# Kernel tuning notes

Hardware: AMD Instinct MI355X
Metric: run time of the kernel (lower is better)

## Reference

```python
import jax, jax.numpy as jnp
import numpy as np

NEG_BIG = -9e15
ALPHA = 0.2  # LeakyReLU slope


def setup_inputs() -> dict:
    key = jax.random.key(0)
    k1, k2, k3, k4 = jax.random.split(key, 4)
    B, N, Fin, Fout = 8, 2048, 256, 64
    h = jax.random.normal(k1, (B, N, Fin), dtype=jnp.float32)
    adj = jax.random.randint(k2, (B, N, N), 0, 2, dtype=jnp.int32)
    # xavier_uniform-ish scale for W and a
    W = jax.random.normal(k3, (Fin, Fout), dtype=jnp.float32) * (1.414 * np.sqrt(2.0 / (Fin + Fout)))
    a = jax.random.normal(k4, (2 * Fout, 1), dtype=jnp.float32) * (1.414 * np.sqrt(2.0 / (2 * Fout + 1)))
    return {"h": h, "adj": adj, "W": W, "a": a}


def reference(h, adj, W, a):
    Fout = W.shape[1]
    Wh = jnp.einsum("bnf,fo->bno", h, W)  # [B,N,Fout]
    # Decompose concat-based score: a_input @ a == Wh@a1 (src) + Wh@a2 (dst)
    a1, a2 = a[:Fout, 0], a[Fout:, 0]
    e_src = Wh @ a1  # [B,N]
    e_dst = Wh @ a2  # [B,N]
    e = e_src[:, :, None] + e_dst[:, None, :]  # [B,N,N]
    e = jnp.where(e > 0, e, ALPHA * e)  # LeakyReLU
    scores = jnp.where(adj > 0, e, NEG_BIG)
    attention = jax.nn.softmax(scores, axis=-1)  # [B,N,N]
    h_prime = jnp.einsum("bnm,bmo->bno", attention, Wh)
    return jax.nn.elu(h_prime)  # concat=True
```

## Files before the change

### kernel.cpp

```cpp
#include <hip/hip_runtime.h>

#define L2E 1.44269504088896340736f

typedef float f32x4 __attribute__((ext_vector_type(4)));
typedef __bf16 bf16x8 __attribute__((ext_vector_type(8)));
typedef __bf16 bf16x4 __attribute__((ext_vector_type(4)));

__device__ inline void mfma_bf16(bf16x8 a, bf16x8 b, f32x4& c) {
    c = __builtin_amdgcn_mfma_f32_16x16x32_bf16(a, b, c, 0, 0, 0);
}

#define WS_ESRC 2097152
#define WS_EDST 2162688
#define WS_NUM  2228224
#define WS_DEN  6422528
#define WS_MSK  6488064


__global__ __launch_bounds__(256, 8)
void k_msk(const int* __restrict__ adj, unsigned* __restrict__ mask) {
    const int t = blockIdx.x * 256 + threadIdx.x;
    const int4* ap = (const int4*)(adj + (size_t)t * 32);
    int4 q0 = ap[0], q1 = ap[1], q2 = ap[2], q3 = ap[3];
    int4 q4 = ap[4], q5 = ap[5], q6 = ap[6], q7 = ap[7];
    unsigned m = 0u;
#define PK(Q, S)                                                              \
    m |= ((Q.x > 0) ? 1u : 0u) << (S);                                        \
    m |= ((Q.y > 0) ? 1u : 0u) << ((S) + 1);                                  \
    m |= ((Q.z > 0) ? 1u : 0u) << ((S) + 2);                                  \
    m |= ((Q.w > 0) ? 1u : 0u) << ((S) + 3);
    PK(q0, 0) PK(q1, 4) PK(q2, 8) PK(q3, 12)
    PK(q4, 16) PK(q5, 20) PK(q6, 24) PK(q7, 28)
#undef PK
    mask[t] = m;
}

__global__ __launch_bounds__(256, 2)
void k1_wh(const float* __restrict__ h, const float* __restrict__ W,
           const float* __restrict__ a, __bf16* __restrict__ whP,
           float* __restrict__ esrc, float* __restrict__ edst,
           float* __restrict__ numden) {
    const int tid  = threadIdx.x;
    const int lane = tid & 63;
    const int w    = tid >> 6;
    const int blk  = blockIdx.x;
    const int r0   = blk * 8;
    const int b    = r0 >> 11;
    const int n0   = r0 & 2047;

    if (tid < 130) {
        const int zi = blk * 130 + tid;
        *(float4*)&numden[zi * 4] = make_float4(0.f, 0.f, 0.f, 0.f);
    }

    __shared__ float pt_s[8][4][64];
    __shared__ float whs[64][8];

    float wreg[64];
    {
        const float* Wp = W + (size_t)(w * 64) * 64 + lane;
#pragma unroll
        for (int kk = 0; kk < 64; kk++) wreg[kk] = Wp[(size_t)kk * 64];
    }

    const float* hbase = h + (size_t)r0 * 256 + w * 64;
    for (int rr = 0; rr < 8; rr++) {
        const float4* hp = (const float4*)(hbase + rr * 256);
        float acc = 0.f;
#pragma unroll
        for (int q = 0; q < 16; q++) {
            float4 hv = hp[q];
            acc += hv.x * wreg[4 * q + 0];
            acc += hv.y * wreg[4 * q + 1];
            acc += hv.z * wreg[4 * q + 2];
            acc += hv.w * wreg[4 * q + 3];
        }
        pt_s[rr][w][lane] = acc;
    }
    __syncthreads();

    const float a1 = a[lane];
    const float a2 = a[64 + lane];
#pragma unroll
    for (int rq = 0; rq < 2; rq++) {
        const int rr = w * 2 + rq;
        float v = pt_s[rr][0][lane] + pt_s[rr][1][lane] +
                  pt_s[rr][2][lane] + pt_s[rr][3][lane];
        whs[lane][rr] = v;
        float e1 = v * a1, e2 = v * a2;
#pragma unroll
        for (int d = 1; d < 64; d <<= 1) {
            e1 += __shfl_xor(e1, d);
            e2 += __shfl_xor(e2, d);
        }
        if (lane == 0) { esrc[r0 + rr] = e1; edst[r0 + rr] = e2; }
    }
    __syncthreads();

    if (tid < 128) {
        const int o  = tid >> 1, hf = (tid & 1) * 4;
        float4 v = *(const float4*)&whs[o][hf];
        bf16x4 bv = { (__bf16)v.x, (__bf16)v.y, (__bf16)v.z, (__bf16)v.w };
        const int t   = n0 >> 6;
        const int kh  = (n0 >> 5) & 1;
        const int hi2 = (n0 >> 3) & 3;
        const int ob  = o >> 4;
        const int rr  = o & 15;
        const size_t flat =
            ((((size_t)(b * 32 + t) * 2 + kh) * 4 + ob) * 4 + hi2) * 128 +
            rr * 8 + hf;
        *(bf16x4*)(whP + flat) = bv;
    }
}

__global__ __launch_bounds__(512, 2)
void k2_attn(const unsigned* __restrict__ mask, const __bf16* __restrict__ whP,
             const float* __restrict__ esrc, const float* __restrict__ edst,
             float* __restrict__ num, float* __restrict__ den) {
    const int tid  = threadIdx.x;
    const int lane = tid & 63;
    const int w    = tid >> 6;
    const int blk  = blockIdx.x;
    const int b    = blk & 7;
    const int t2   = blk >> 3;
    const int jq   = t2 & 3;
    const int rg   = t2 >> 2;
    const int i0   = rg * 128;
    const int r    = lane & 15;
    const int hi   = lane >> 4;

    __shared__ __align__(16) __bf16 whp_s[32768];
    __shared__ unsigned msk_s[128][18];
    __shared__ float edst_s[512];
    __shared__ float esrc_s[128];
    __shared__ float red_s[8];

    const __bf16* wsrc = whP + (size_t)b * 131072 + (size_t)jq * 32768;
#pragma unroll
    for (int it = 0; it < 8; it++) {
        const int idx = it * 512 + tid;
        *(bf16x8*)&whp_s[idx * 8] = *(const bf16x8*)&wsrc[(size_t)idx * 8];
    }
    const unsigned* mbase = mask + (size_t)(b * 2048 + i0) * 64 + jq * 16;
#pragma unroll
    for (int it = 0; it < 4; it++) {
        const int idx  = it * 512 + tid;
        const int rloc = idx >> 4;
        const int wloc = idx & 15;
        msk_s[rloc][wloc] = mbase[(size_t)rloc * 64 + wloc];
    }
    {
        float4 v = *(const float4*)&edst[b * 2048 + tid * 4];
        float mymax = fmaxf(fmaxf(v.x, v.y), fmaxf(v.z, v.w));
#pragma unroll
        for (int d = 1; d < 64; d <<= 1)
            mymax = fmaxf(mymax, __shfl_xor(mymax, d));
        if (lane == 0) red_s[w] = mymax;
    }
    edst_s[tid] = edst[b * 2048 + jq * 512 + tid];
    if (tid < 128) esrc_s[tid] = esrc[b * 2048 + i0 + tid];
    __syncthreads();

    float maxed = red_s[0];
#pragma unroll
    for (int q = 1; q < 8; q++) maxed = fmaxf(maxed, red_s[q]);
    const float es = esrc_s[w * 16 + r];
    float M = es + maxed;
    M = fmaxf(M, 0.2f * M);
    const float Mc = M * L2E;

    f32x4 lacc = {0.f, 0.f, 0.f, 0.f};
    f32x4 acc0 = {0,0,0,0}, acc1 = {0,0,0,0}, acc2 = {0,0,0,0}, acc3 = {0,0,0,0};

#define PB(E, bits, sh, base)                                                 \
    {                                                                         \
        const unsigned bb = (bits) >> (sh);                                   \
        float v;                                                              \
        v = es + E.x; v = fmaxf(v, 0.2f * v);                                 \
        p[base + 0] = (bb & 1u) ? exp2f(__builtin_fmaf(v, L2E, -Mc)) : 0.f;   \
        v = es + E.y; v = fmaxf(v, 0.2f * v);                                 \
        p[base + 1] = (bb & 2u) ? exp2f(__builtin_fmaf(v, L2E, -Mc)) : 0.f;   \
        v = es + E.z; v = fmaxf(v, 0.2f * v);                                 \
        p[base + 2] = (bb & 4u) ? exp2f(__builtin_fmaf(v, L2E, -Mc)) : 0.f;   \
        v = es + E.w; v = fmaxf(v, 0.2f * v);                                 \
        p[base + 3] = (bb & 8u) ? exp2f(__builtin_fmaf(v, L2E, -Mc)) : 0.f;   \
    }

    for (int tl = 0; tl < 8; ++tl) {
        const int jt = tl * 64;
        const uint2 m2 = *(const uint2*)&msk_s[w * 16 + r][tl * 2];
        const unsigned aLo = m2.x >> (hi * 8);
        const unsigned aHi = m2.y >> (hi * 8);
        const __bf16* wb = whp_s + tl * 4096 + lane * 8;
        bf16x8 B00 = *(const bf16x8*)(wb);
        bf16x8 B01 = *(const bf16x8*)(wb + 512);
        bf16x8 B02 = *(const bf16x8*)(wb + 1024);
        bf16x8 B03 = *(const bf16x8*)(wb + 1536);
        bf16x8 B10 = *(const bf16x8*)(wb + 2048);
        bf16x8 B11 = *(const bf16x8*)(wb + 2560);
        bf16x8 B12 = *(const bf16x8*)(wb + 3072);
        bf16x8 B13 = *(const bf16x8*)(wb + 3584);
        float4 e0 = *(const float4*)&edst_s[jt + hi * 8];
        float4 e1 = *(const float4*)&edst_s[jt + hi * 8 + 4];
        float4 e2 = *(const float4*)&edst_s[jt + 32 + hi * 8];
        float4 e3 = *(const float4*)&edst_s[jt + 32 + hi * 8 + 4];
        float p[16];
        PB(e0, aLo, 0, 0) PB(e1, aLo, 4, 4) PB(e2, aHi, 0, 8) PB(e3, aHi, 4, 12)
        lacc[0] += p[0] + p[4] + p[8]  + p[12];
        lacc[1] += p[1] + p[5] + p[9]  + p[13];
        lacc[2] += p[2] + p[6] + p[10] + p[14];
        lacc[3] += p[3] + p[7] + p[11] + p[15];
        bf16x8 pa0, pa1;
#pragma unroll
        for (int e = 0; e < 8; e++) {
            pa0[e] = (__bf16)p[e];
            pa1[e] = (__bf16)p[e + 8];
        }
        mfma_bf16(pa0, B00, acc0); mfma_bf16(pa1, B10, acc0);
        mfma_bf16(pa0, B01, acc1); mfma_bf16(pa1, B11, acc1);
        mfma_bf16(pa0, B02, acc2); mfma_bf16(pa1, B12, acc2);
        mfma_bf16(pa0, B03, acc3); mfma_bf16(pa1, B13, acc3);
    }
#undef PB

    float lsum = lacc[0] + lacc[1] + lacc[2] + lacc[3];
    lsum += __shfl_xor(lsum, 16);
    lsum += __shfl_xor(lsum, 32);
    const int rowbase = b * 2048 + i0 + w * 16;
    if (lane < 16) atomicAdd(&den[rowbase + r], lsum);
#pragma unroll
    for (int reg = 0; reg < 4; reg++) {
        float* np = num + (size_t)(rowbase + 4 * hi + reg) * 64 + r;
        atomicAdd(np +  0, acc0[reg]);
        atomicAdd(np + 16, acc1[reg]);
        atomicAdd(np + 32, acc2[reg]);
        atomicAdd(np + 48, acc3[reg]);
    }
}

__global__ __launch_bounds__(256, 4)
void k3_fin(const float* __restrict__ num, const float* __restrict__ den,
            float* __restrict__ out) {
    const int i = blockIdx.x * 256 + threadIdx.x;
    float4 n = *(const float4*)&num[(size_t)i * 4];
    const float inv = 1.0f / den[i >> 4];
    float v0 = n.x * inv, v1 = n.y * inv, v2 = n.z * inv, v3 = n.w * inv;
    v0 = v0 > 0.f ? v0 : expm1f(v0);
    v1 = v1 > 0.f ? v1 : expm1f(v1);
    v2 = v2 > 0.f ? v2 : expm1f(v2);
    v3 = v3 > 0.f ? v3 : expm1f(v3);
    *(float4*)&out[(size_t)i * 4] = make_float4(v0, v1, v2, v3);
}

extern "C" void kernel_launch(void* const* d_in, const int* in_sizes, int n_in,
                              void* d_out, int out_size, void* d_ws, size_t ws_size,
                              hipStream_t stream) {
    const float* h   = (const float*)d_in[0];
    const int*   adj = (const int*)d_in[1];
    const float* W   = (const float*)d_in[2];
    const float* a   = (const float*)d_in[3];
    float* out = (float*)d_out;

    char* ws = (char*)d_ws;
    __bf16*   whP  = (__bf16*)ws;
    float*    esrc = (float*)(ws + WS_ESRC);
    float*    edst = (float*)(ws + WS_EDST);
    float*    num  = (float*)(ws + WS_NUM);
    float*    den  = (float*)(ws + WS_DEN);
    unsigned* mask = (unsigned*)(ws + WS_MSK);

    hipLaunchKernelGGL(k_msk, dim3(4096), dim3(256), 0, stream, adj, mask);
    hipLaunchKernelGGL(k1_wh, dim3(2048), dim3(256), 0, stream,
                       h, W, a, whP, esrc, edst, num);
    hipLaunchKernelGGL(k2_attn, dim3(512), dim3(512), 0, stream,
                       mask, whP, esrc, edst, num, den);
    hipLaunchKernelGGL(k3_fin, dim3(1024), dim3(256), 0, stream,
                       num, den, out);
}
```

Before: 86.04 us.

## Coalesce adjacency mask packing and replace atomics with per-chunk partial buffers

The mask-packing kernel now has each wave read the adjacency rows with lane-contiguous int4 loads. It then rearranges the packed nibbles through shared memory so the output bit order is preserved. The attention kernel writes its numerator and denominator partials into separate per-column-chunk buffers instead of using atomicAdd. The finalize kernel sums the four partials, which also removes the zeroing pass from the Wh kernel. This costs extra workspace and extra partial-buffer traffic in the finalize step.

```diff
diff --git a/kernel.cpp b/kernel.cpp
--- a/kernel.cpp
+++ b/kernel.cpp
@@ -12,34 +12,47 @@
 
 #define WS_ESRC 2097152
 #define WS_EDST 2162688
-#define WS_NUM  2228224
-#define WS_DEN  6422528
-#define WS_MSK  6488064
+#define WS_MSK  2228224
+#define WS_NUM  6422528
+#define WS_DEN  23199744
 
 
 __global__ __launch_bounds__(256, 8)
 void k_msk(const int* __restrict__ adj, unsigned* __restrict__ mask) {
-    const int t = blockIdx.x * 256 + threadIdx.x;
-    const int4* ap = (const int4*)(adj + (size_t)t * 32);
-    int4 q0 = ap[0], q1 = ap[1], q2 = ap[2], q3 = ap[3];
-    int4 q4 = ap[4], q5 = ap[5], q6 = ap[6], q7 = ap[7];
-    unsigned m = 0u;
-#define PK(Q, S)                                                              \
-    m |= ((Q.x > 0) ? 1u : 0u) << (S);                                        \
-    m |= ((Q.y > 0) ? 1u : 0u) << ((S) + 1);                                  \
-    m |= ((Q.z > 0) ? 1u : 0u) << ((S) + 2);                                  \
-    m |= ((Q.w > 0) ? 1u : 0u) << ((S) + 3);
-    PK(q0, 0) PK(q1, 4) PK(q2, 8) PK(q3, 12)
-    PK(q4, 16) PK(q5, 20) PK(q6, 24) PK(q7, 28)
-#undef PK
-    mask[t] = m;
+    __shared__ unsigned pk_s[4][64];
+    const int lane = threadIdx.x & 63;
+    const int wv   = threadIdx.x >> 6;
+    const int gw   = blockIdx.x * 4 + wv;
+    for (int cc = 0; cc < 4; cc++) {
+        const int c = gw * 4 + cc;
+        const int4* ap = (const int4*)adj + (size_t)c * 512 + lane;
+        int4 v[8];
+#pragma unroll
+        for (int q = 0; q < 8; q++) v[q] = ap[q * 64];
+        unsigned wl = 0u;
+#pragma unroll
+        for (int q = 0; q < 8; q++) {
+            unsigned nib = (v[q].x > 0 ? 1u : 0u) | (v[q].y > 0 ? 2u : 0u) |
+                           (v[q].z > 0 ? 4u : 0u) | (v[q].w > 0 ? 8u : 0u);
+            wl |= nib << (4 * q);
+        }
+        pk_s[wv][lane] = wl;
+        unsigned W[8];
+        *(uint4*)&W[0] = *(const uint4*)&pk_s[wv][8 * (lane & 7)];
+        *(uint4*)&W[4] = *(const uint4*)&pk_s[wv][8 * (lane & 7) + 4];
+        const int qsel = 4 * (lane >> 3);
+        unsigned ow = 0u;
+#pragma unroll
+        for (int i2 = 0; i2 < 8; i2++)
+            ow |= ((W[i2] >> qsel) & 0xFu) << (4 * i2);
+        mask[(size_t)c * 64 + lane] = ow;
+    }
 }
 
 __global__ __launch_bounds__(256, 2)
 void k1_wh(const float* __restrict__ h, const float* __restrict__ W,
            const float* __restrict__ a, __bf16* __restrict__ whP,
-           float* __restrict__ esrc, float* __restrict__ edst,
-           float* __restrict__ numden) {
+           float* __restrict__ esrc, float* __restrict__ edst) {
     const int tid  = threadIdx.x;
     const int lane = tid & 63;
     const int w    = tid >> 6;
@@ -47,11 +60,6 @@
     const int r0   = blk * 8;
     const int b    = r0 >> 11;
     const int n0   = r0 & 2047;
-
-    if (tid < 130) {
-        const int zi = blk * 130 + tid;
-        *(float4*)&numden[zi * 4] = make_float4(0.f, 0.f, 0.f, 0.f);
-    }
 
     __shared__ float pt_s[8][4][64];
     __shared__ float whs[64][8];
@@ -116,7 +124,7 @@
 __global__ __launch_bounds__(512, 2)
 void k2_attn(const unsigned* __restrict__ mask, const __bf16* __restrict__ whP,
              const float* __restrict__ esrc, const float* __restrict__ edst,
-             float* __restrict__ num, float* __restrict__ den) {
+             float* __restrict__ nump, float* __restrict__ denp) {
     const int tid  = threadIdx.x;
     const int lane = tid & 63;
     const int w    = tid >> 6;
@@ -227,24 +235,31 @@
     lsum += __shfl_xor(lsum, 16);
     lsum += __shfl_xor(lsum, 32);
     const int rowbase = b * 2048 + i0 + w * 16;
-    if (lane < 16) atomicAdd(&den[rowbase + r], lsum);
+    if (lane < 16) denp[jq * 16384 + rowbase + r] = lsum;
+    float* npq = nump + (size_t)jq * 1048576;
 #pragma unroll
     for (int reg = 0; reg < 4; reg++) {
-        float* np = num + (size_t)(rowbase + 4 * hi + reg) * 64 + r;
-        atomicAdd(np +  0, acc0[reg]);
-        atomicAdd(np + 16, acc1[reg]);
-        atomicAdd(np + 32, acc2[reg]);
-        atomicAdd(np + 48, acc3[reg]);
+        float* np = npq + (size_t)(rowbase + 4 * hi + reg) * 64 + r;
+        np[0]  = acc0[reg];
+        np[16] = acc1[reg];
+        np[32] = acc2[reg];
+        np[48] = acc3[reg];
     }
 }
 
 __global__ __launch_bounds__(256, 4)
-void k3_fin(const float* __restrict__ num, const float* __restrict__ den,
+void k3_fin(const float* __restrict__ nump, const float* __restrict__ denp,
             float* __restrict__ out) {
     const int i = blockIdx.x * 256 + threadIdx.x;
-    float4 n = *(const float4*)&num[(size_t)i * 4];
-    const float inv = 1.0f / den[i >> 4];
-    float v0 = n.x * inv, v1 = n.y * inv, v2 = n.z * inv, v3 = n.w * inv;
+    f32x4 n = *(const f32x4*)&nump[(size_t)i * 4];
+    n += *(const f32x4*)&nump[1048576 + (size_t)i * 4];
+    n += *(const f32x4*)&nump[2097152 + (size_t)i * 4];
+    n += *(const f32x4*)&nump[3145728 + (size_t)i * 4];
+    const int row = i >> 4;
+    const float d = denp[row] + denp[16384 + row] +
+                    denp[32768 + row] + denp[49152 + row];
+    const float inv = 1.0f / d;
+    float v0 = n[0] * inv, v1 = n[1] * inv, v2 = n[2] * inv, v3 = n[3] * inv;
     v0 = v0 > 0.f ? v0 : expm1f(v0);
     v1 = v1 > 0.f ? v1 : expm1f(v1);
     v2 = v2 > 0.f ? v2 : expm1f(v2);
@@ -265,15 +280,15 @@
     __bf16*   whP  = (__bf16*)ws;
     float*    esrc = (float*)(ws + WS_ESRC);
     float*    edst = (float*)(ws + WS_EDST);
-    float*    num  = (float*)(ws + WS_NUM);
-    float*    den  = (float*)(ws + WS_DEN);
     unsigned* mask = (unsigned*)(ws + WS_MSK);
-
-    hipLaunchKernelGGL(k_msk, dim3(4096), dim3(256), 0, stream, adj, mask);
+    float*    nump = (float*)(ws + WS_NUM);
+    float*    denp = (float*)(ws + WS_DEN);
+
+    hipLaunchKernelGGL(k_msk, dim3(1024), dim3(256), 0, stream, adj, mask);
     hipLaunchKernelGGL(k1_wh, dim3(2048), dim3(256), 0, stream,
-                       h, W, a, whP, esrc, edst, num);
+                       h, W, a, whP, esrc, edst);
     hipLaunchKernelGGL(k2_attn, dim3(512), dim3(512), 0, stream,
-                       mask, whP, esrc, edst, num, den);
+                       mask, whP, esrc, edst, nump, denp);
     hipLaunchKernelGGL(k3_fin, dim3(1024), dim3(256), 0, stream,
-                       num, den, out);
-}
+                       nump, denp, out);
+}
```

Measured after the change: 86.68 us. Within noise of the previous version (+0.7%).
